# Optimization experiments

Hardware: AMD Instinct MI355X
Metric: run time of the kernel (lower is better)

Reference implementation:

```python
import jax, jax.numpy as jnp
import numpy as np

B, C, H, W = 4, 64, 64, 64  # prompt and kv share the same BCHW shape
EPS = 1e-5
OFR = 4.0  # offset_range_factor
SCALE = (C // 1) ** -0.5  # n_head_channels = dim / n_heads = 64


def conv1x1(x, w, b=None):
    y = jnp.einsum('oc,bchw->bohw', w, x)
    if b is not None:
        y = y + b[None, :, None, None]
    return y


def grid_sample_bilinear(img, grid):
    # img: [N,C,Hp,Wp], grid: [N,Hg,Wg,2] with (x,y) in [-1,1], align_corners=True, zeros padding
    N, Cc, Hp, Wp = img.shape
    Hg, Wg = grid.shape[1], grid.shape[2]
    gx = (grid[..., 0] + 1.0) * 0.5 * (Wp - 1)
    gy = (grid[..., 1] + 1.0) * 0.5 * (Hp - 1)
    x0 = jnp.floor(gx)
    y0 = jnp.floor(gy)
    img_f = img.reshape(N, Cc, Hp * Wp)

    def gather(xi, yi):
        valid = (xi >= 0) & (xi <= Wp - 1) & (yi >= 0) & (yi <= Hp - 1)
        xi_c = jnp.clip(xi, 0, Wp - 1).astype(jnp.int32)
        yi_c = jnp.clip(yi, 0, Hp - 1).astype(jnp.int32)
        idx = (yi_c * Wp + xi_c).reshape(N, 1, -1)
        vals = jnp.take_along_axis(img_f, idx, axis=2)  # [N,C,Hg*Wg]
        return vals, valid.reshape(N, 1, -1).astype(img.dtype)

    v00, m00 = gather(x0, y0)
    v01, m01 = gather(x0 + 1, y0)
    v10, m10 = gather(x0, y0 + 1)
    v11, m11 = gather(x0 + 1, y0 + 1)
    wx = (gx - x0).reshape(N, 1, -1)
    wy = (gy - y0).reshape(N, 1, -1)
    out = (v00 * m00 * (1 - wx) * (1 - wy) + v01 * m01 * wx * (1 - wy)
           + v10 * m10 * (1 - wx) * wy + v11 * m11 * wx * wy)
    return out.reshape(N, Cc, Hg, Wg)


def setup_inputs() -> dict:
    key = jax.random.key(0)
    ks = jax.random.split(key, 8)
    s = 0.02
    return {
        'prompt': jax.random.normal(ks[0], (B, C, H, W), jnp.float32),
        'kv': jax.random.normal(ks[1], (B, C, H, W), jnp.float32),
        'wq': s * jax.random.normal(ks[2], (C, C), jnp.float32),
        'bq': jnp.zeros((C,), jnp.float32),
        'wk': s * jax.random.normal(ks[3], (C, C), jnp.float32),
        'bk': jnp.zeros((C,), jnp.float32),
        'wv': s * jax.random.normal(ks[4], (C, C), jnp.float32),
        'bv': jnp.zeros((C,), jnp.float32),
        'wo': s * jax.random.normal(ks[5], (C, C), jnp.float32),
        'bo': jnp.zeros((C,), jnp.float32),
        'dw_w': s * jax.random.normal(ks[6], (C, 1, 3, 3), jnp.float32),  # depthwise 3x3
        'dw_b': jnp.zeros((C,), jnp.float32),
        'ln_w': jnp.ones((C,), jnp.float32),
        'ln_b': jnp.zeros((C,), jnp.float32),
        'off_w': s * jax.random.normal(ks[7], (2, C), jnp.float32),  # 1x1 conv to 2 offset channels
    }


def reference(prompt, kv, wq, bq, wk, bk, wv, bv, wo, bo, dw_w, dw_b, ln_w, ln_b, off_w):
    # q projection (n_groups=1 so group view == full view)
    q = conv1x1(prompt, wq, bq)  # [B,C,H,W]

    # conv_offset: depthwise 3x3 -> WithBias LayerNorm over channels -> GELU -> 1x1 to 2ch
    t = jax.lax.conv_general_dilated(q, dw_w, (1, 1), ((1, 1), (1, 1)),
                                     feature_group_count=C)
    t = t + dw_b[None, :, None, None]
    mu = t.mean(axis=1, keepdims=True)
    var = t.var(axis=1, keepdims=True)
    t = (t - mu) / jnp.sqrt(var + EPS) * ln_w[None, :, None, None] + ln_b[None, :, None, None]
    t = jax.nn.gelu(t, approximate=False)
    offset = jnp.einsum('oc,bchw->bohw', off_w, t)  # [B,2,H,W] (y,x) channels

    Hk, Wk = offset.shape[2], offset.shape[3]
    n = Hk * Wk
    rng = jnp.array([1.0 / (Hk - 1.0), 1.0 / (Wk - 1.0)], dtype=offset.dtype).reshape(1, 2, 1, 1)
    offset = jnp.tanh(offset) * rng * OFR
    offset = jnp.transpose(offset, (0, 2, 3, 1))  # [B,Hk,Wk,2] (y,x)

    ref_y = (jnp.linspace(0.5, Hk - 0.5, Hk) / (Hk - 1.0)) * 2.0 - 1.0
    ref_x = (jnp.linspace(0.5, Wk - 0.5, Wk) / (Wk - 1.0)) * 2.0 - 1.0
    ry, rx = jnp.meshgrid(ref_y, ref_x, indexing='ij')
    ref = jnp.stack((ry, rx), axis=-1)[None].astype(offset.dtype)  # [1,Hk,Wk,2]

    pos = offset + ref
    grid = pos[..., ::-1]  # swap to (x,y)
    xs = grid_sample_bilinear(kv, grid)  # [B,C,Hk,Wk]
    xs = xs.reshape(B, C, n)

    k = jnp.einsum('oc,bcn->bon', wk, xs) + bk[None, :, None]
    v = jnp.einsum('oc,bcn->bon', wv, xs) + bv[None, :, None]
    qf = q.reshape(B, C, H * W)

    attn = jnp.einsum('bcm,bcn->bmn', qf, k) * SCALE  # [B,HW,n]
    attn = jax.nn.softmax(attn, axis=2)
    out = jnp.einsum('bmn,bcn->bcm', attn, v).reshape(B, C, H, W)
    return conv1x1(out, wo, bo)
```

## Files before the change

### kernel.cpp

```cpp
#include <hip/hip_runtime.h>
#include <math.h>

#define BB 4
#define CC 64
#define HH 64
#define WW 64
#define HWP 4096
#define NPTS 4096
#define NSPLIT 4
#define LDP 72
constexpr float K_EPS   = 1e-5f;
constexpr float K_OFR   = 4.0f;

#define QF_OFF  0
#define QB_OFF  1048576
#define GXY_OFF 1572864
#define KB_OFF  1605632
#define VB_OFF  2129920
#define OP_OFF  2654208
#define DP_OFF  3702784

typedef short frag8 __attribute__((ext_vector_type(8)));
typedef float f32x4 __attribute__((ext_vector_type(4)));

static __device__ inline unsigned short f2bf(float f) {
  unsigned int u = __builtin_bit_cast(unsigned int, f);
  unsigned int r = (u + 0x7fffu + ((u >> 16) & 1u)) >> 16;
  return (unsigned short)r;
}

__global__ __launch_bounds__(512) void k_qproj(
    const float* __restrict__ prompt, const float* __restrict__ wq,
    const float* __restrict__ bq, float* __restrict__ qf,
    unsigned short* __restrict__ qb) {
  __shared__ float w_s[64 * 64];
  __shared__ float p_s[64 * 64];
  __shared__ unsigned short t_s[64 * 68];
  int tid = threadIdx.x;
  int blk = blockIdx.x;
  int b = blk >> 6; int hw0 = (blk & 63) * 64;
#pragma unroll
  for (int i = 0; i < 8; ++i) w_s[i * 512 + tid] = wq[i * 512 + tid];
#pragma unroll
  for (int i = 0; i < 8; ++i) {
    int idx = i * 512 + tid; int c = idx >> 6, pix = idx & 63;
    p_s[idx] = prompt[(size_t)(b * CC + c) * HWP + hw0 + pix];
  }
  __syncthreads();
  int x = tid & 63, og = tid >> 6;
  float acc[8];
#pragma unroll
  for (int oo = 0; oo < 8; ++oo) acc[oo] = bq[og * 8 + oo];
  for (int cg = 0; cg < 16; ++cg) {
    float p0 = p_s[(cg * 4 + 0) * 64 + x];
    float p1 = p_s[(cg * 4 + 1) * 64 + x];
    float p2 = p_s[(cg * 4 + 2) * 64 + x];
    float p3 = p_s[(cg * 4 + 3) * 64 + x];
#pragma unroll
    for (int oo = 0; oo < 8; ++oo) {
      const float4 w4 = *(const float4*)&w_s[(og * 8 + oo) * 64 + cg * 4];
      acc[oo] = fmaf(w4.x, p0, fmaf(w4.y, p1, fmaf(w4.z, p2, fmaf(w4.w, p3, acc[oo]))));
    }
  }
#pragma unroll
  for (int oo = 0; oo < 8; ++oo) {
    int o = og * 8 + oo;
    qf[(size_t)(b * CC + o) * HWP + hw0 + x] = acc[oo];
    t_s[x * 68 + o] = f2bf(acc[oo] * 0.125f);
  }
  __syncthreads();
#pragma unroll
  for (int i = 0; i < 2; ++i) {
    int idx = i * 512 + tid;
    int pix = idx >> 4, c4 = idx & 15;
    ushort4 v = *(const ushort4*)&t_s[pix * 68 + c4 * 4];
    *(ushort4*)&qb[(size_t)(b * HWP + hw0 + pix) * CC + c4 * 4] = v;
  }
}

__global__ __launch_bounds__(512) void k_offsets(
    const float* __restrict__ q, const float* __restrict__ dw_w,
    const float* __restrict__ dw_b, const float* __restrict__ ln_w,
    const float* __restrict__ ln_b, const float* __restrict__ off_w,
    float* __restrict__ gxy) {
  int tid = threadIdx.x;
  int x = tid & 63;
  int cg = tid >> 6;
  int by = blockIdx.x;
  int b = by >> 6;
  int y = by & 63;

  __shared__ float red0[8][64];
  __shared__ float red1[8][64];

  float t[8];
#pragma unroll
  for (int i = 0; i < 8; ++i) {
    int c = cg * 8 + i;
    float acc = dw_b[c];
    const float* qc = q + (size_t)(b * CC + c) * HWP;
#pragma unroll
    for (int ky = 0; ky < 3; ++ky) {
      int yy = y + ky - 1;
      bool yok = (yy >= 0) && (yy < HH);
#pragma unroll
      for (int kx = 0; kx < 3; ++kx) {
        int xx = x + kx - 1;
        bool ok = yok && (xx >= 0) && (xx < WW);
        float v = ok ? qc[yy * WW + xx] : 0.f;
        acc = fmaf(dw_w[c * 9 + ky * 3 + kx], v, acc);
      }
    }
    t[i] = acc;
  }
  float s1 = 0.f, s2 = 0.f;
#pragma unroll
  for (int i = 0; i < 8; ++i) { s1 += t[i]; s2 += t[i] * t[i]; }
  red0[cg][x] = s1;
  red1[cg][x] = s2;
  __syncthreads();
  float mu = 0.f, ms = 0.f;
#pragma unroll
  for (int g = 0; g < 8; ++g) { mu += red0[g][x]; ms += red1[g][x]; }
  mu *= (1.f / 64.f); ms *= (1.f / 64.f);
  float rstd = rsqrtf(ms - mu * mu + K_EPS);

  float oy = 0.f, ox = 0.f;
#pragma unroll
  for (int i = 0; i < 8; ++i) {
    int c = cg * 8 + i;
    float g = (t[i] - mu) * rstd * ln_w[c] + ln_b[c];
    g = 0.5f * g * (1.f + erff(g * 0.70710678118654752f));
    oy = fmaf(off_w[c], g, oy);
    ox = fmaf(off_w[CC + c], g, ox);
  }
  __syncthreads();
  red0[cg][x] = oy;
  red1[cg][x] = ox;
  __syncthreads();
  if (cg == 0) {
    float osy = 0.f, osx = 0.f;
#pragma unroll
    for (int g = 0; g < 8; ++g) { osy += red0[g][x]; osx += red1[g][x]; }
    osy = tanhf(osy) * (K_OFR / (HH - 1));
    osx = tanhf(osx) * (K_OFR / (WW - 1));
    float ry = (y + 0.5f) * (2.f / 63.f) - 1.f;
    float rx = (x + 0.5f) * (2.f / 63.f) - 1.f;
    float gx = (osx + rx + 1.f) * 0.5f * (WW - 1);
    float gy = (osy + ry + 1.f) * 0.5f * (HH - 1);
    int n = y * WW + x;
    gxy[(b * HWP + n) * 2 + 0] = gx;
    gxy[(b * HWP + n) * 2 + 1] = gy;
  }
}

__global__ __launch_bounds__(512) void k_sample_kv(
    const float* __restrict__ kv, const float* __restrict__ gxy,
    const float* __restrict__ wk, const float* __restrict__ bk,
    const float* __restrict__ wv, const float* __restrict__ bv,
    unsigned short* __restrict__ kb, unsigned short* __restrict__ vb) {
  __shared__ float wk_s[64 * 64];
  __shared__ float wv_s[64 * 64];
  __shared__ float xs_s[64 * 64];
  int tid = threadIdx.x;
  int blk = blockIdx.x;
  int b = blk >> 6; int n0 = (blk & 63) * 64;
#pragma unroll
  for (int i = 0; i < 8; ++i) {
    wk_s[i * 512 + tid] = wk[i * 512 + tid];
    wv_s[i * 512 + tid] = wv[i * 512 + tid];
  }
  int n = tid & 63, og = tid >> 6;
  int p = b * HWP + n0 + n;
  float gx = gxy[p * 2 + 0], gy = gxy[p * 2 + 1];
  float x0f = floorf(gx), y0f = floorf(gy);
  float wx = gx - x0f, wy = gy - y0f;
  int x0 = (int)x0f, y0 = (int)y0f;
  int x1 = x0 + 1, y1 = y0 + 1;
  float m00 = (x0 >= 0 && x0 < WW && y0 >= 0 && y0 < HH) ? 1.f : 0.f;
  float m01 = (x1 >= 0 && x1 < WW && y0 >= 0 && y0 < HH) ? 1.f : 0.f;
  float m10 = (x0 >= 0 && x0 < WW && y1 >= 0 && y1 < HH) ? 1.f : 0.f;
  float m11 = (x1 >= 0 && x1 < WW && y1 >= 0 && y1 < HH) ? 1.f : 0.f;
  int x0c = min(max(x0, 0), WW - 1), x1c = min(max(x1, 0), WW - 1);
  int y0c = min(max(y0, 0), HH - 1), y1c = min(max(y1, 0), HH - 1);
  int i00 = y0c * WW + x0c, i01 = y0c * WW + x1c;
  int i10 = y1c * WW + x0c, i11 = y1c * WW + x1c;
  float w00 = m00 * (1.f - wx) * (1.f - wy);
  float w01 = m01 * wx * (1.f - wy);
  float w10 = m10 * (1.f - wx) * wy;
  float w11 = m11 * wx * wy;

  const float* base = kv + (size_t)b * CC * HWP;
#pragma unroll
  for (int i = 0; i < 8; ++i) {
    int c = og * 8 + i;
    const float* pc = base + (size_t)c * HWP;
    xs_s[c * 64 + n] = w00 * pc[i00] + w01 * pc[i01] + w10 * pc[i10] + w11 * pc[i11];
  }
  __syncthreads();
  float ak[8], av[8];
#pragma unroll
  for (int oo = 0; oo < 8; ++oo) { ak[oo] = bk[og * 8 + oo]; av[oo] = bv[og * 8 + oo]; }
  for (int cg = 0; cg < 16; ++cg) {
    float p0 = xs_s[(cg * 4 + 0) * 64 + n];
    float p1 = xs_s[(cg * 4 + 1) * 64 + n];
    float p2 = xs_s[(cg * 4 + 2) * 64 + n];
    float p3 = xs_s[(cg * 4 + 3) * 64 + n];
#pragma unroll
    for (int oo = 0; oo < 8; ++oo) {
      int o = og * 8 + oo;
      const float4 k4 = *(const float4*)&wk_s[o * 64 + cg * 4];
      const float4 v4 = *(const float4*)&wv_s[o * 64 + cg * 4];
      ak[oo] = fmaf(k4.x, p0, fmaf(k4.y, p1, fmaf(k4.z, p2, fmaf(k4.w, p3, ak[oo]))));
      av[oo] = fmaf(v4.x, p0, fmaf(v4.y, p1, fmaf(v4.z, p2, fmaf(v4.w, p3, av[oo]))));
    }
  }
  unsigned short tk[8];
#pragma unroll
  for (int oo = 0; oo < 8; ++oo) tk[oo] = f2bf(ak[oo]);
  size_t krow = (size_t)(b * NPTS + n0 + n) * CC + og * 8;
  *(uint4*)&kb[krow] = *(const uint4*)&tk[0];
#pragma unroll
  for (int oo = 0; oo < 8; ++oo) {
    int o = og * 8 + oo;
    vb[(size_t)(b * CC + o) * NPTS + n0 + n] = f2bf(av[oo]);
  }
}

__global__ __launch_bounds__(256) void k_attn(
    const unsigned short* __restrict__ qb, const unsigned short* __restrict__ kb,
    const unsigned short* __restrict__ vb, float* __restrict__ opart,
    float* __restrict__ dpart) {
  __shared__ short qp_s[64 * LDP];
  __shared__ short k_s[64 * LDP];
  __shared__ short v_s[64 * LDP];

  int tid = threadIdx.x;
  int w = tid >> 6, lane = tid & 63, quad = lane >> 4, l16 = lane & 15;
  int blk = blockIdx.x;
  int mt = blk & 63; int bns = blk >> 6; int ns = bns & 3; int b = bns >> 2;
  int m0 = mt * 64;

  const unsigned short* qbb = qb + (size_t)b * HWP * CC;
  const unsigned short* kbb = kb + (size_t)b * NPTS * CC;
  const unsigned short* vbb = vb + (size_t)b * CC * NPTS;

#pragma unroll
  for (int pass = 0; pass < 2; ++pass) {
    int idx = pass * 256 + tid;
    int row = idx >> 3, part = idx & 7;
    uint4 d = *(const uint4*)(qbb + (size_t)(m0 + row) * CC + part * 8);
    *(uint4*)&qp_s[row * LDP + part * 8] = d;
  }
  __syncthreads();
  frag8 a_frag[2];
#pragma unroll
  for (int kc = 0; kc < 2; ++kc)
    a_frag[kc] = *(const frag8*)&qp_s[(w * 16 + l16) * LDP + kc * 32 + quad * 8];

  f32x4 o_acc[4];
  float d_acc[4];
#pragma unroll
  for (int i = 0; i < 4; ++i) {
    d_acc[i] = 0.f;
    o_acc[i][0] = 0.f; o_acc[i][1] = 0.f; o_acc[i][2] = 0.f; o_acc[i][3] = 0.f;
  }

  int nbase = ns * (NPTS / NSPLIT);
  for (int it = 0; it < (NPTS / NSPLIT) / 64; ++it) {
    int n0 = nbase + it * 64;
    __syncthreads();
#pragma unroll
    for (int pass = 0; pass < 2; ++pass) {
      int idx = pass * 256 + tid;
      int row = idx >> 3, part = idx & 7;
      uint4 dk = *(const uint4*)(kbb + (size_t)(n0 + row) * CC + part * 8);
      uint4 dv = *(const uint4*)(vbb + (size_t)row * NPTS + n0 + part * 8);
      *(uint4*)&k_s[row * LDP + part * 8] = dk;
      *(uint4*)&v_s[row * LDP + part * 8] = dv;
    }
    __syncthreads();

    f32x4 s_acc[4];
#pragma unroll
    for (int t = 0; t < 4; ++t) {
      s_acc[t][0] = 0.f; s_acc[t][1] = 0.f; s_acc[t][2] = 0.f; s_acc[t][3] = 0.f;
    }
#pragma unroll
    for (int kc = 0; kc < 2; ++kc) {
#pragma unroll
      for (int t = 0; t < 4; ++t) {
        frag8 bf = *(const frag8*)&k_s[(t * 16 + l16) * LDP + kc * 32 + quad * 8];
        s_acc[t] = __builtin_amdgcn_mfma_f32_16x16x32_bf16(a_frag[kc], bf, s_acc[t], 0, 0, 0);
      }
    }
#pragma unroll
    for (int t = 0; t < 4; ++t) {
#pragma unroll
      for (int r = 0; r < 4; ++r) {
        float pv = __expf(s_acc[t][r]);
        unsigned short ph = f2bf(pv);
        qp_s[(w * 16 + quad * 4 + r) * LDP + t * 16 + l16] = (short)ph;
        d_acc[r] += __builtin_bit_cast(float, (unsigned int)ph << 16);
      }
    }
#pragma unroll
    for (int kc = 0; kc < 2; ++kc) {
      frag8 bp = *(const frag8*)&qp_s[(w * 16 + l16) * LDP + kc * 32 + quad * 8];
#pragma unroll
      for (int ct = 0; ct < 4; ++ct) {
        frag8 av = *(const frag8*)&v_s[(ct * 16 + l16) * LDP + kc * 32 + quad * 8];
        o_acc[ct] = __builtin_amdgcn_mfma_f32_16x16x32_bf16(av, bp, o_acc[ct], 0, 0, 0);
      }
    }
  }

  float* op = opart + (size_t)b * HWP * CC + (size_t)(m0 + w * 16 + l16) * CC;
#pragma unroll
  for (int ct = 0; ct < 4; ++ct) {
#pragma unroll
    for (int r = 0; r < 4; ++r)
      unsafeAtomicAdd(&op[ct * 16 + quad * 4 + r], o_acc[ct][r]);
  }
#pragma unroll
  for (int r = 0; r < 4; ++r) {
    float d = d_acc[r];
    d += __shfl_xor(d, 1); d += __shfl_xor(d, 2);
    d += __shfl_xor(d, 4); d += __shfl_xor(d, 8);
    if (l16 == 0)
      unsafeAtomicAdd(&dpart[b * HWP + m0 + w * 16 + quad * 4 + r], d);
  }
}

__global__ __launch_bounds__(256) void k_out(
    const float* __restrict__ opart, const float* __restrict__ dpart,
    const float* __restrict__ wo, const float* __restrict__ bo,
    float* __restrict__ out) {
  __shared__ float wo_s[CC * CC];
  __shared__ float t_s[64 * 65];
  int tid = threadIdx.x;
  int blk = blockIdx.x;
  int b = blk >> 6, mt = blk & 63, m0 = mt * 64;
  for (int i = tid; i < CC * CC; i += 256) wo_s[i] = wo[i];

  const float* o0 = opart + (size_t)b * HWP * CC;
  const float* d0 = dpart + b * HWP;
#pragma unroll
  for (int it = 0; it < 16; ++it) {
    int idx = it * 256 + tid;
    int m = idx >> 6, c = idx & 63;
    float denom = d0[m0 + m];
    t_s[m * 65 + c] = o0[(size_t)(m0 + m) * CC + c] / denom;
  }
  __syncthreads();
  int ml = tid & 63, og = tid >> 6;
  for (int oo = 0; oo < 16; ++oo) {
    int o = og * 16 + oo;
    float acc = bo[o];
#pragma unroll
    for (int c = 0; c < 64; ++c) acc = fmaf(wo_s[o * CC + c], t_s[ml * 65 + c], acc);
    out[(size_t)(b * CC + o) * HWP + m0 + ml] = acc;
  }
}

extern "C" void kernel_launch(void* const* d_in, const int* in_sizes, int n_in,
                              void* d_out, int out_size, void* d_ws, size_t ws_size,
                              hipStream_t stream) {
  const float* prompt = (const float*)d_in[0];
  const float* kv     = (const float*)d_in[1];
  const float* wq     = (const float*)d_in[2];
  const float* bq     = (const float*)d_in[3];
  const float* wk     = (const float*)d_in[4];
  const float* bk     = (const float*)d_in[5];
  const float* wv     = (const float*)d_in[6];
  const float* bv     = (const float*)d_in[7];
  const float* wo     = (const float*)d_in[8];
  const float* bo     = (const float*)d_in[9];
  const float* dw_w   = (const float*)d_in[10];
  const float* dw_b   = (const float*)d_in[11];
  const float* ln_w   = (const float*)d_in[12];
  const float* ln_b   = (const float*)d_in[13];
  const float* off_w  = (const float*)d_in[14];
  float* out = (float*)d_out;
  float* ws  = (float*)d_ws;

  float* qf             = ws + QF_OFF;
  unsigned short* qb    = (unsigned short*)(ws + QB_OFF);
  float* gxy            = ws + GXY_OFF;
  unsigned short* kb    = (unsigned short*)(ws + KB_OFF);
  unsigned short* vb    = (unsigned short*)(ws + VB_OFF);
  float* opart          = ws + OP_OFF;
  float* dpart          = ws + DP_OFF;

  hipMemsetAsync(opart, 0, (size_t)(1048576 + 16384) * sizeof(float), stream);

  hipLaunchKernelGGL(k_qproj, dim3(BB * 64), dim3(512), 0, stream,
                     prompt, wq, bq, qf, qb);
  hipLaunchKernelGGL(k_offsets, dim3(BB * HH), dim3(512), 0, stream,
                     qf, dw_w, dw_b, ln_w, ln_b, off_w, gxy);
  hipLaunchKernelGGL(k_sample_kv, dim3(BB * 64), dim3(512), 0, stream,
                     kv, gxy, wk, bk, wv, bv, kb, vb);
  hipLaunchKernelGGL(k_attn, dim3(BB * NSPLIT * 64), dim3(256), 0, stream,
                     qb, kb, vb, opart, dpart);
  hipLaunchKernelGGL(k_out, dim3(BB * 64), dim3(256), 0, stream,
                     opart, dpart, wo, bo, out);
}
```

Measured before the change: 202.3 us.

## Fuse offset and KV sampling kernels, replace atomics with per-split partials

Merges the offset-generation and KV bilinear-sampling/projection kernels into one, passing the sampling grid through shared memory instead of a global buffer. The attention kernel now writes each split's partial outputs and denominators to separate buffers with plain vector stores. The final kernel sums these partials, which removes the memset and the float atomics. The softmax uses exp2 with log2(e) folded into the query scale. The workspace layout is reorganized: qf aliases the partial buffer, and the split count depends on workspace size. The cost is a larger workspace and extra partial reads in the output kernel.

```diff
diff --git a/kernel.cpp b/kernel.cpp
--- a/kernel.cpp
+++ b/kernel.cpp
@@ -7,18 +7,11 @@
 #define WW 64
 #define HWP 4096
 #define NPTS 4096
-#define NSPLIT 4
 #define LDP 72
 constexpr float K_EPS   = 1e-5f;
 constexpr float K_OFR   = 4.0f;
-
-#define QF_OFF  0
-#define QB_OFF  1048576
-#define GXY_OFF 1572864
-#define KB_OFF  1605632
-#define VB_OFF  2129920
-#define OP_OFF  2654208
-#define DP_OFF  3702784
+constexpr float K_QSCALE = 0.18033688011112042f;
+
 
 typedef short frag8 __attribute__((ext_vector_type(8)));
 typedef float f32x4 __attribute__((ext_vector_type(4)));
@@ -66,7 +59,7 @@
   for (int oo = 0; oo < 8; ++oo) {
     int o = og * 8 + oo;
     qf[(size_t)(b * CC + o) * HWP + hw0 + x] = acc[oo];
-    t_s[x * 68 + o] = f2bf(acc[oo] * 0.125f);
+    t_s[x * 68 + o] = f2bf(acc[oo] * K_QSCALE);
   }
   __syncthreads();
 #pragma unroll
@@ -78,11 +71,20 @@
   }
 }
 
-__global__ __launch_bounds__(512) void k_offsets(
+__global__ __launch_bounds__(512) void k_off_sample(
     const float* __restrict__ q, const float* __restrict__ dw_w,
     const float* __restrict__ dw_b, const float* __restrict__ ln_w,
     const float* __restrict__ ln_b, const float* __restrict__ off_w,
-    float* __restrict__ gxy) {
+    const float* __restrict__ kv,
+    const float* __restrict__ wk, const float* __restrict__ bk,
+    const float* __restrict__ wv, const float* __restrict__ bv,
+    unsigned short* __restrict__ kb, unsigned short* __restrict__ vb) {
+  __shared__ float wk_s[64 * 64];
+  __shared__ float wv_s[64 * 64];
+  __shared__ float xs_s[64 * 64];
+  __shared__ float red0[8][64];
+  __shared__ float red1[8][64];
+
   int tid = threadIdx.x;
   int x = tid & 63;
   int cg = tid >> 6;
@@ -90,8 +92,11 @@
   int b = by >> 6;
   int y = by & 63;
 
-  __shared__ float red0[8][64];
-  __shared__ float red1[8][64];
+#pragma unroll
+  for (int i = 0; i < 8; ++i) {
+    wk_s[i * 512 + tid] = wk[i * 512 + tid];
+    wv_s[i * 512 + tid] = wv[i * 512 + tid];
+  }
 
   float t[8];
 #pragma unroll
@@ -146,33 +151,14 @@
     osx = tanhf(osx) * (K_OFR / (WW - 1));
     float ry = (y + 0.5f) * (2.f / 63.f) - 1.f;
     float rx = (x + 0.5f) * (2.f / 63.f) - 1.f;
-    float gx = (osx + rx + 1.f) * 0.5f * (WW - 1);
-    float gy = (osy + ry + 1.f) * 0.5f * (HH - 1);
-    int n = y * WW + x;
-    gxy[(b * HWP + n) * 2 + 0] = gx;
-    gxy[(b * HWP + n) * 2 + 1] = gy;
-  }
-}
-
-__global__ __launch_bounds__(512) void k_sample_kv(
-    const float* __restrict__ kv, const float* __restrict__ gxy,
-    const float* __restrict__ wk, const float* __restrict__ bk,
-    const float* __restrict__ wv, const float* __restrict__ bv,
-    unsigned short* __restrict__ kb, unsigned short* __restrict__ vb) {
-  __shared__ float wk_s[64 * 64];
-  __shared__ float wv_s[64 * 64];
-  __shared__ float xs_s[64 * 64];
-  int tid = threadIdx.x;
-  int blk = blockIdx.x;
-  int b = blk >> 6; int n0 = (blk & 63) * 64;
-#pragma unroll
-  for (int i = 0; i < 8; ++i) {
-    wk_s[i * 512 + tid] = wk[i * 512 + tid];
-    wv_s[i * 512 + tid] = wv[i * 512 + tid];
-  }
-  int n = tid & 63, og = tid >> 6;
-  int p = b * HWP + n0 + n;
-  float gx = gxy[p * 2 + 0], gy = gxy[p * 2 + 1];
+    red0[0][x] = (osx + rx + 1.f) * 0.5f * (WW - 1);
+    red0[1][x] = (osy + ry + 1.f) * 0.5f * (HH - 1);
+  }
+  __syncthreads();
+
+  int n = x, og = cg;
+  int n0 = y * 64;
+  float gx = red0[0][n], gy = red0[1][n];
   float x0f = floorf(gx), y0f = floorf(gy);
   float wx = gx - x0f, wy = gy - y0f;
   int x0 = (int)x0f, y0 = (int)y0f;
@@ -201,16 +187,16 @@
   float ak[8], av[8];
 #pragma unroll
   for (int oo = 0; oo < 8; ++oo) { ak[oo] = bk[og * 8 + oo]; av[oo] = bv[og * 8 + oo]; }
-  for (int cg = 0; cg < 16; ++cg) {
-    float p0 = xs_s[(cg * 4 + 0) * 64 + n];
-    float p1 = xs_s[(cg * 4 + 1) * 64 + n];
-    float p2 = xs_s[(cg * 4 + 2) * 64 + n];
-    float p3 = xs_s[(cg * 4 + 3) * 64 + n];
+  for (int cg2 = 0; cg2 < 16; ++cg2) {
+    float p0 = xs_s[(cg2 * 4 + 0) * 64 + n];
+    float p1 = xs_s[(cg2 * 4 + 1) * 64 + n];
+    float p2 = xs_s[(cg2 * 4 + 2) * 64 + n];
+    float p3 = xs_s[(cg2 * 4 + 3) * 64 + n];
 #pragma unroll
     for (int oo = 0; oo < 8; ++oo) {
       int o = og * 8 + oo;
-      const float4 k4 = *(const float4*)&wk_s[o * 64 + cg * 4];
-      const float4 v4 = *(const float4*)&wv_s[o * 64 + cg * 4];
+      const float4 k4 = *(const float4*)&wk_s[o * 64 + cg2 * 4];
+      const float4 v4 = *(const float4*)&wv_s[o * 64 + cg2 * 4];
       ak[oo] = fmaf(k4.x, p0, fmaf(k4.y, p1, fmaf(k4.z, p2, fmaf(k4.w, p3, ak[oo]))));
       av[oo] = fmaf(v4.x, p0, fmaf(v4.y, p1, fmaf(v4.z, p2, fmaf(v4.w, p3, av[oo]))));
     }
@@ -230,7 +216,7 @@
 __global__ __launch_bounds__(256) void k_attn(
     const unsigned short* __restrict__ qb, const unsigned short* __restrict__ kb,
     const unsigned short* __restrict__ vb, float* __restrict__ opart,
-    float* __restrict__ dpart) {
+    float* __restrict__ dpart, int ns_shift) {
   __shared__ short qp_s[64 * LDP];
   __shared__ short k_s[64 * LDP];
   __shared__ short v_s[64 * LDP];
@@ -238,7 +224,8 @@
   int tid = threadIdx.x;
   int w = tid >> 6, lane = tid & 63, quad = lane >> 4, l16 = lane & 15;
   int blk = blockIdx.x;
-  int mt = blk & 63; int bns = blk >> 6; int ns = bns & 3; int b = bns >> 2;
+  int mt = blk & 63; int bns = blk >> 6;
+  int ns = bns & ((1 << ns_shift) - 1); int b = bns >> ns_shift;
   int m0 = mt * 64;
 
   const unsigned short* qbb = qb + (size_t)b * HWP * CC;
@@ -266,8 +253,9 @@
     o_acc[i][0] = 0.f; o_acc[i][1] = 0.f; o_acc[i][2] = 0.f; o_acc[i][3] = 0.f;
   }
 
-  int nbase = ns * (NPTS / NSPLIT);
-  for (int it = 0; it < (NPTS / NSPLIT) / 64; ++it) {
+  int niters = (NPTS / 64) >> ns_shift;
+  int nbase = ns * niters * 64;
+  for (int it = 0; it < niters; ++it) {
     int n0 = nbase + it * 64;
     __syncthreads();
 #pragma unroll
@@ -298,7 +286,7 @@
     for (int t = 0; t < 4; ++t) {
 #pragma unroll
       for (int r = 0; r < 4; ++r) {
-        float pv = __expf(s_acc[t][r]);
+        float pv = exp2f(s_acc[t][r]);
         unsigned short ph = f2bf(pv);
         qp_s[(w * 16 + quad * 4 + r) * LDP + t * 16 + l16] = (short)ph;
         d_acc[r] += __builtin_bit_cast(float, (unsigned int)ph << 16);
@@ -315,12 +303,12 @@
     }
   }
 
-  float* op = opart + (size_t)b * HWP * CC + (size_t)(m0 + w * 16 + l16) * CC;
+  float* op = opart + (size_t)((ns * BB + b) * HWP + m0 + w * 16 + l16) * CC;
 #pragma unroll
   for (int ct = 0; ct < 4; ++ct) {
-#pragma unroll
-    for (int r = 0; r < 4; ++r)
-      unsafeAtomicAdd(&op[ct * 16 + quad * 4 + r], o_acc[ct][r]);
+    float4 o4;
+    o4.x = o_acc[ct][0]; o4.y = o_acc[ct][1]; o4.z = o_acc[ct][2]; o4.w = o_acc[ct][3];
+    *(float4*)&op[ct * 16 + quad * 4] = o4;
   }
 #pragma unroll
   for (int r = 0; r < 4; ++r) {
@@ -328,14 +316,14 @@
     d += __shfl_xor(d, 1); d += __shfl_xor(d, 2);
     d += __shfl_xor(d, 4); d += __shfl_xor(d, 8);
     if (l16 == 0)
-      unsafeAtomicAdd(&dpart[b * HWP + m0 + w * 16 + quad * 4 + r], d);
+      dpart[(ns * BB + b) * HWP + m0 + w * 16 + quad * 4 + r] = d;
   }
 }
 
 __global__ __launch_bounds__(256) void k_out(
     const float* __restrict__ opart, const float* __restrict__ dpart,
     const float* __restrict__ wo, const float* __restrict__ bo,
-    float* __restrict__ out) {
+    float* __restrict__ out, int NS) {
   __shared__ float wo_s[CC * CC];
   __shared__ float t_s[64 * 65];
   int tid = threadIdx.x;
@@ -343,14 +331,16 @@
   int b = blk >> 6, mt = blk & 63, m0 = mt * 64;
   for (int i = tid; i < CC * CC; i += 256) wo_s[i] = wo[i];
 
-  const float* o0 = opart + (size_t)b * HWP * CC;
-  const float* d0 = dpart + b * HWP;
 #pragma unroll
   for (int it = 0; it < 16; ++it) {
     int idx = it * 256 + tid;
     int m = idx >> 6, c = idx & 63;
-    float denom = d0[m0 + m];
-    t_s[m * 65 + c] = o0[(size_t)(m0 + m) * CC + c] / denom;
+    float o = 0.f, d = 0.f;
+    for (int s = 0; s < NS; ++s) {
+      o += opart[(size_t)((s * BB + b) * HWP + m0 + m) * CC + c];
+      d += dpart[(s * BB + b) * HWP + m0 + m];
+    }
+    t_s[m * 65 + c] = o / d;
   }
   __syncthreads();
   int ml = tid & 63, og = tid >> 6;
@@ -384,24 +374,24 @@
   float* out = (float*)d_out;
   float* ws  = (float*)d_ws;
 
-  float* qf             = ws + QF_OFF;
-  unsigned short* qb    = (unsigned short*)(ws + QB_OFF);
-  float* gxy            = ws + GXY_OFF;
-  unsigned short* kb    = (unsigned short*)(ws + KB_OFF);
-  unsigned short* vb    = (unsigned short*)(ws + VB_OFF);
-  float* opart          = ws + OP_OFF;
-  float* dpart          = ws + DP_OFF;
-
-  hipMemsetAsync(opart, 0, (size_t)(1048576 + 16384) * sizeof(float), stream);
+  const size_t need4 = (size_t)(4 * 1048576 + 3 * 524288 + 4 * 16384) * sizeof(float);
+  int NS, ns_shift;
+  if (ws_size >= need4) { NS = 4; ns_shift = 2; } else { NS = 2; ns_shift = 1; }
+
+  float* opart          = ws;
+  float* qf             = ws;
+  unsigned short* qb    = (unsigned short*)(ws + (size_t)NS * 1048576);
+  unsigned short* kb    = (unsigned short*)(ws + (size_t)NS * 1048576 + 524288);
+  unsigned short* vb    = (unsigned short*)(ws + (size_t)NS * 1048576 + 2 * 524288);
+  float* dpart          = ws + (size_t)NS * 1048576 + 3 * 524288;
 
   hipLaunchKernelGGL(k_qproj, dim3(BB * 64), dim3(512), 0, stream,
                      prompt, wq, bq, qf, qb);
-  hipLaunchKernelGGL(k_offsets, dim3(BB * HH), dim3(512), 0, stream,
-                     qf, dw_w, dw_b, ln_w, ln_b, off_w, gxy);
-  hipLaunchKernelGGL(k_sample_kv, dim3(BB * 64), dim3(512), 0, stream,
-                     kv, gxy, wk, bk, wv, bv, kb, vb);
-  hipLaunchKernelGGL(k_attn, dim3(BB * NSPLIT * 64), dim3(256), 0, stream,
-                     qb, kb, vb, opart, dpart);
+  hipLaunchKernelGGL(k_off_sample, dim3(BB * HH), dim3(512), 0, stream,
+                     qf, dw_w, dw_b, ln_w, ln_b, off_w,
+                     kv, wk, bk, wv, bv, kb, vb);
+  hipLaunchKernelGGL(k_attn, dim3(BB * NS * 64), dim3(256), 0, stream,
+                     qb, kb, vb, opart, dpart, ns_shift);
   hipLaunchKernelGGL(k_out, dim3(BB * 64), dim3(256), 0, stream,
-                     opart, dpart, wo, bo, out);
-}
+                     opart, dpart, wo, bo, out, NS);
+}
```

After: 177.7 us. -12.1%, faster.
